# Performance work log

Hardware: AMD Instinct MI355X
Metric: run time of the kernel (lower is better)

The kernel has to match this reference:

```python
import jax, jax.numpy as jnp
import numpy as np

BLOCK = 64       # _aether_cfg['block_size']
JL_DIM = 32      # epsilon_jl_bridge d_out
EPS_GOV = 0.5    # fixed governor eps (governor.target)
ROPE_BASE = 10000.0
RMS_EPS = 1e-6


def _normalize(x, axis=-1):
    n = jnp.sqrt(jnp.sum(x * x, axis=axis, keepdims=True))
    return x / jnp.maximum(n, 1e-12)


def _rms_norm(x):
    return x * jax.lax.rsqrt(jnp.mean(x * x, axis=-1, keepdims=True) + RMS_EPS)


def _rope(x, cos, sin):
    half = x.shape[-1] // 2
    x1, x2 = x[..., :half], x[..., half:]
    return jnp.concatenate([x1 * cos + x2 * sin, -x1 * sin + x2 * cos], axis=-1)


def setup_inputs() -> dict:
    key = jax.random.key(0)
    ks = jax.random.split(key, 6)
    B, S, Dm, H = 2, 2048, 2048, 16
    sc = 1.0 / np.sqrt(Dm)
    x = jax.random.normal(ks[0], (B, S, Dm), jnp.float32)
    Wq = jax.random.normal(ks[1], (Dm, Dm), jnp.float32) * sc
    Wk = jax.random.normal(ks[2], (Dm, Dm), jnp.float32) * sc
    Wv = jax.random.normal(ks[3], (Dm, Dm), jnp.float32) * sc
    Wo = jax.random.normal(ks[4], (Dm, Dm), jnp.float32) * sc
    q_gain = jnp.ones((H,), jnp.float32)
    return {"x": x, "Wq": Wq, "Wk": Wk, "Wv": Wv, "Wo": Wo, "q_gain": q_gain}


def reference(x, Wq, Wk, Wv, Wo, q_gain):
    B, S, Dm = x.shape
    H = q_gain.shape[0]
    Dh = Dm // H

    # QKV projections (bias-free linear, torch weight layout [out,in])
    q = (x @ Wq.T).reshape(B, S, H, Dh).transpose(0, 2, 1, 3)  # (B,H,S,Dh)
    k = (x @ Wk.T).reshape(B, S, H, Dh).transpose(0, 2, 1, 3)
    v = (x @ Wv.T).reshape(B, S, H, Dh).transpose(0, 2, 1, 3)

    # RoPE tables
    inv_freq = 1.0 / (ROPE_BASE ** (jnp.arange(0, Dh, 2, dtype=jnp.float32) / Dh))
    freqs = jnp.outer(jnp.arange(S, dtype=jnp.float32), inv_freq)  # (S,Dh/2)
    cos = jnp.cos(freqs)[None, None]
    sin = jnp.sin(freqs)[None, None]

    q = _rope(_rms_norm(q), cos, sin) * q_gain[None, :, None, None]
    k = _rope(_rms_norm(k), cos, sin)

    # --- aether sparse SDPA: JL block bounds -> top-k blocks -> gather -> SDPA ---
    N = S // BLOCK  # number of KV blocks (static)
    proj = jax.random.normal(jax.random.key(42), (Dh, JL_DIM), jnp.float32) / np.sqrt(JL_DIM)

    q_proj = _normalize(q.mean(axis=2, keepdims=True) @ proj)          # (B,H,1,JL)
    k_blocks = k.reshape(B, H, N, BLOCK, Dh)
    k_proj = _normalize(k_blocks @ proj)                               # (B,H,N,BLOCK,JL)
    centroids = _normalize(k_proj.mean(axis=3))                        # (B,H,N,JL)
    radii = jnp.clip(
        1.0 - jnp.min(jnp.sum(k_proj * centroids[:, :, :, None, :], axis=-1), axis=-1),
        0.0, 1.0)                                                      # (B,H,N)
    ub = jnp.einsum('bhqj,bhnj->bhqn', q_proj, centroids) + radii[:, :, None, :]
    scores = ub[:, :, 0, :]                                            # (B,H,N)
    # force-include the last two blocks (union in the original code)
    scores = scores.at[:, :, N - 2:].set(jnp.inf)

    n_keep = max(2, int(N * min(1.0, EPS_GOV))) + 2                    # static
    _, top_idx = jax.lax.top_k(scores, n_keep)                         # (B,H,n_keep)
    top_idx = jnp.sort(top_idx, axis=-1)
    idx = (top_idx[..., None] * BLOCK + jnp.arange(BLOCK)).reshape(B, H, -1)  # (B,H,K)

    k_s = jnp.take_along_axis(k, idx[..., None], axis=2)               # (B,H,K,Dh)
    v_s = jnp.take_along_axis(v, idx[..., None], axis=2)

    att = jax.nn.softmax(
        jnp.einsum('bhqd,bhkd->bhqk', q, k_s) / np.sqrt(Dh), axis=-1)  # (B,H,S,K)
    y = jnp.einsum('bhqk,bhkd->bhqd', att, v_s)                        # (B,H,S,Dh)

    y = y.transpose(0, 2, 1, 3).reshape(B, S, Dm)
    return y @ Wo.T
```

## Files before the change

kernel.cpp:

```cpp
#include <hip/hip_runtime.h>
#include <hip/hip_bf16.h>

#define B_ 2
#define S_ 2048
#define DM 2048
#define H_ 16
#define DH 128
#define NBLK 32
#define NKEEP 18
#define BH (B_ * H_)

typedef __attribute__((ext_vector_type(8))) short short8;
typedef __attribute__((ext_vector_type(8))) _Float16 f16x8;
typedef __attribute__((ext_vector_type(4))) _Float16 f16x4;
typedef __attribute__((ext_vector_type(4))) float f32x4;

#define GLOAD16(gp, lp)                                                        \
  __builtin_amdgcn_global_load_lds(                                            \
      (const __attribute__((address_space(1))) unsigned int*)(const void*)(gp),\
      (__attribute__((address_space(3))) unsigned int*)(void*)(lp), 16, 0, 0)

__device__ __forceinline__ unsigned short f32_to_bf16(float f) {
  unsigned u = __float_as_uint(f);
  unsigned r = (u + 0x7fffu + ((u >> 16) & 1u)) >> 16;
  return (unsigned short)r;
}
__device__ __forceinline__ float bf16_to_f32(unsigned short h) {
  return __uint_as_float(((unsigned)h) << 16);
}

__device__ __forceinline__ unsigned rotl32(unsigned x, int r) {
  return (x << r) | (x >> (32 - r));
}

__device__ __forceinline__ float erfinv_f32(float x) {
  float w = -log1pf(-x * x);
  float p;
  if (w < 5.0f) {
    w -= 2.5f;
    p = 2.81022636e-08f;
    p = fmaf(p, w, 3.43273939e-07f);
    p = fmaf(p, w, -3.5233877e-06f);
    p = fmaf(p, w, -4.39150654e-06f);
    p = fmaf(p, w, 0.00021858087f);
    p = fmaf(p, w, -0.00125372503f);
    p = fmaf(p, w, -0.00417768164f);
    p = fmaf(p, w, 0.246640727f);
    p = fmaf(p, w, 1.50140941f);
  } else {
    w = sqrtf(w) - 3.0f;
    p = -0.000200214257f;
    p = fmaf(p, w, 0.000100950558f);
    p = fmaf(p, w, 0.00134934322f);
    p = fmaf(p, w, -0.00367342844f);
    p = fmaf(p, w, 0.00573950773f);
    p = fmaf(p, w, -0.0076224613f);
    p = fmaf(p, w, 0.00943887047f);
    p = fmaf(p, w, 1.00167406f);
    p = fmaf(p, w, 2.83297682f);
  }
  return p * x;
}

__device__ __forceinline__ float bits_to_normal(unsigned b) {
  float f = __uint_as_float((b >> 9) | 0x3f800000u) - 1.0f;
  const float lo = -0.9999999403953552f;
  float u = fmaxf(lo, fmaf(f, 2.0f, lo));
  return 1.4142135623730951f * erfinv_f32(u);
}

__global__ void proj_kernel(float* __restrict__ proj) {
  int i = blockIdx.x * blockDim.x + threadIdx.x;
  if (i >= 4096) return;
  unsigned k0 = 0u, k1 = 42u;
  unsigned k2 = 0x1BD11BDAu ^ k0 ^ k1;
  unsigned x0 = 0u, x1 = (unsigned)i;
  x0 += k0; x1 += k1;
#define QR(r) { x0 += x1; x1 = rotl32(x1, r); x1 ^= x0; }
  QR(13) QR(15) QR(26) QR(6)   x0 += k1; x1 += k2 + 1u;
  QR(17) QR(29) QR(16) QR(24)  x0 += k2; x1 += k0 + 2u;
  QR(13) QR(15) QR(26) QR(6)   x0 += k0; x1 += k1 + 3u;
  QR(17) QR(29) QR(16) QR(24)  x0 += k1; x1 += k2 + 4u;
  QR(13) QR(15) QR(26) QR(6)   x0 += k2; x1 += k0 + 5u;
#undef QR
  proj[i] = bits_to_normal(x0 ^ x1) / 5.656854249492381f;
}

__global__ void rope_table_kernel(float* __restrict__ cosb, float* __restrict__ sinb) {
  int s = blockIdx.x;
  int j = threadIdx.x;
  double e = (double)(2 * j) / 128.0;
  double invf = 1.0 / pow(10000.0, e);
  float freq = (float)s * (float)invf;
  cosb[s * 64 + j] = (float)cos((double)freq);
  sinb[s * 64 + j] = (float)sin((double)freq);
}

__global__ __launch_bounds__(256) void split_x3_kernel(const float* __restrict__ in,
                                                       unsigned short* __restrict__ hi,
                                                       unsigned short* __restrict__ lo,
                                                       _Float16* __restrict__ f16,
                                                       int n4) {
  int i = blockIdx.x * blockDim.x + threadIdx.x;
  if (i >= n4) return;
  float4 v = ((const float4*)in)[i];
  ushort4 hv, lv;
  f16x4 fv;
  hv.x = f32_to_bf16(v.x); lv.x = f32_to_bf16(v.x - bf16_to_f32(hv.x)); fv[0] = (_Float16)v.x;
  hv.y = f32_to_bf16(v.y); lv.y = f32_to_bf16(v.y - bf16_to_f32(hv.y)); fv[1] = (_Float16)v.y;
  hv.z = f32_to_bf16(v.z); lv.z = f32_to_bf16(v.z - bf16_to_f32(hv.z)); fv[2] = (_Float16)v.z;
  hv.w = f32_to_bf16(v.w); lv.w = f32_to_bf16(v.w - bf16_to_f32(hv.w)); fv[3] = (_Float16)v.w;
  ((ushort4*)hi)[i] = hv;
  ((ushort4*)lo)[i] = lv;
  ((f16x4*)f16)[i] = fv;
}

__global__ __launch_bounds__(256) void split_kernel(const float* __restrict__ in,
                                                    unsigned short* __restrict__ hi,
                                                    unsigned short* __restrict__ lo,
                                                    int n4) {
  int i = blockIdx.x * blockDim.x + threadIdx.x;
  if (i >= n4) return;
  float4 v = ((const float4*)in)[i];
  ushort4 hv, lv;
  hv.x = f32_to_bf16(v.x); lv.x = f32_to_bf16(v.x - bf16_to_f32(hv.x));
  hv.y = f32_to_bf16(v.y); lv.y = f32_to_bf16(v.y - bf16_to_f32(hv.y));
  hv.z = f32_to_bf16(v.z); lv.z = f32_to_bf16(v.z - bf16_to_f32(hv.z));
  hv.w = f32_to_bf16(v.w); lv.w = f32_to_bf16(v.w - bf16_to_f32(hv.w));
  ((ushort4*)hi)[i] = hv;
  ((ushort4*)lo)[i] = lv;
}

__global__ __launch_bounds__(256) void split_f16_kernel(const float* __restrict__ in,
                                                        _Float16* __restrict__ f16,
                                                        int n4) {
  int i = blockIdx.x * blockDim.x + threadIdx.x;
  if (i >= n4) return;
  float4 v = ((const float4*)in)[i];
  f16x4 fv;
  fv[0] = (_Float16)v.x; fv[1] = (_Float16)v.y;
  fv[2] = (_Float16)v.z; fv[3] = (_Float16)v.w;
  ((f16x4*)f16)[i] = fv;
}

__global__ __launch_bounds__(512, 2) void mfma_gemm_k_sk(const unsigned short* __restrict__ Ahi,
                                                         const unsigned short* __restrict__ Alo,
                                                         const unsigned short* __restrict__ Whi,
                                                         const unsigned short* __restrict__ Wlo,
                                                         float* __restrict__ kp0,
                                                         float* __restrict__ kp1) {
  __shared__ char smem[131072];
  const int t = threadIdx.x, l = t & 63, w = t >> 6;
  const int lin = blockIdx.z * 128 + blockIdx.y * 8 + blockIdx.x;
  const int swz = (lin & 7) * 32 + (lin >> 3);
  const int kz = swz >> 7;
  const int idx = swz & 127;
  const int n0 = (idx & 7) * 256;
  const int m0 = (idx >> 3) * 256;
  const int kbase = kz * 1024;
  float* C = kz ? kp1 : kp0;
  const int wm = w >> 2, wn = w & 3;
  const int lr = l & 15;
  const int lg8 = (l >> 4) * 8;
  const size_t rstep = (size_t)16 * DM;

  const unsigned short* gAh = Ahi + (size_t)(m0 + w * 32 + lr) * DM + lg8;
  const unsigned short* gAl = Alo + (size_t)(m0 + w * 32 + lr) * DM + lg8;
  const unsigned short* gBh = Whi + (size_t)(n0 + w * 32 + lr) * DM + lg8;
  const unsigned short* gBl = Wlo + (size_t)(n0 + w * 32 + lr) * DM + lg8;

  f32x4 acc[8][4];
#pragma unroll
  for (int i = 0; i < 8; ++i)
#pragma unroll
    for (int j = 0; j < 4; ++j) acc[i][j] = (f32x4){0.f, 0.f, 0.f, 0.f};

  {
    char* base = smem + w * 2048;
    GLOAD16(gAh + kbase, base);
    GLOAD16(gAh + rstep + kbase, base + 1024);
    GLOAD16(gAl + kbase, base + 16384);
    GLOAD16(gAl + rstep + kbase, base + 16384 + 1024);
    GLOAD16(gBh + kbase, base + 32768);
    GLOAD16(gBh + rstep + kbase, base + 32768 + 1024);
    GLOAD16(gBl + kbase, base + 49152);
    GLOAD16(gBl + rstep + kbase, base + 49152 + 1024);
  }
  int cur = 0;

#define KQUAD(q)                                                                        \
  {                                                                                     \
    short8 ah0 = *(const short8*)(buf + (wm * 8 + 2 * (q)) * 1024 + l * 16);            \
    short8 ah1 = *(const short8*)(buf + (wm * 8 + 2 * (q) + 1) * 1024 + l * 16);        \
    short8 al0 = *(const short8*)(buf + 16384 + (wm * 8 + 2 * (q)) * 1024 + l * 16);    \
    short8 al1 = *(const short8*)(buf + 16384 + (wm * 8 + 2 * (q) + 1) * 1024 + l * 16);\
    __builtin_amdgcn_s_setprio(1);                                                      \
    _Pragma("unroll")                                                                   \
    for (int n = 0; n < 4; ++n) {                                                       \
      acc[2 * (q)][n] = __builtin_amdgcn_mfma_f32_16x16x32_bf16(ah0, bh[n], acc[2 * (q)][n], 0, 0, 0); \
      acc[2 * (q)][n] = __builtin_amdgcn_mfma_f32_16x16x32_bf16(ah0, bl[n], acc[2 * (q)][n], 0, 0, 0); \
      acc[2 * (q)][n] = __builtin_amdgcn_mfma_f32_16x16x32_bf16(al0, bh[n], acc[2 * (q)][n], 0, 0, 0); \
    }                                                                                   \
    _Pragma("unroll")                                                                   \
    for (int n = 0; n < 4; ++n) {                                                       \
      acc[2 * (q) + 1][n] = __builtin_amdgcn_mfma_f32_16x16x32_bf16(ah1, bh[n], acc[2 * (q) + 1][n], 0, 0, 0); \
      acc[2 * (q) + 1][n] = __builtin_amdgcn_mfma_f32_16x16x32_bf16(ah1, bl[n], acc[2 * (q) + 1][n], 0, 0, 0); \
      acc[2 * (q) + 1][n] = __builtin_amdgcn_mfma_f32_16x16x32_bf16(al1, bh[n], acc[2 * (q) + 1][n], 0, 0, 0); \
    }                                                                                   \
    __builtin_amdgcn_s_setprio(0);                                                      \
  }

  for (int k0 = kbase; k0 < kbase + 1024; k0 += 32) {
    const bool more = (k0 + 32 < kbase + 1024);
    char* buf = smem + cur * 65536;
    char* nb = smem + (cur ^ 1) * 65536 + w * 2048;
    const int kn = k0 + 32;

    if (more) {
      GLOAD16(gBh + kn, nb + 32768);
      GLOAD16(gBh + rstep + kn, nb + 32768 + 1024);
      asm volatile("s_waitcnt vmcnt(2)" ::: "memory");
    } else {
      asm volatile("s_waitcnt vmcnt(0)" ::: "memory");
    }
    __builtin_amdgcn_s_barrier();

    short8 bh[4], bl[4];
#pragma unroll
    for (int f = 0; f < 4; ++f) {
      bh[f] = *(const short8*)(buf + 32768 + (wn * 4 + f) * 1024 + l * 16);
      bl[f] = *(const short8*)(buf + 49152 + (wn * 4 + f) * 1024 + l * 16);
    }
    KQUAD(0);
    __builtin_amdgcn_s_barrier();

    if (more) {
      GLOAD16(gBl + kn, nb + 49152);
      GLOAD16(gBl + rstep + kn, nb + 49152 + 1024);
    }
    KQUAD(1);
    __builtin_amdgcn_s_barrier();

    if (more) {
      GLOAD16(gAh + kn, nb);
      GLOAD16(gAh + rstep + kn, nb + 1024);
    }
    KQUAD(2);
    __builtin_amdgcn_s_barrier();

    if (more) {
      GLOAD16(gAl + kn, nb + 16384);
      GLOAD16(gAl + rstep + kn, nb + 16384 + 1024);
    }
    KQUAD(3);
    __builtin_amdgcn_s_barrier();

    cur ^= 1;
  }
#undef KQUAD

#pragma unroll
  for (int m = 0; m < 8; ++m) {
    int row0 = m0 + wm * 128 + m * 16 + (l >> 4) * 4;
#pragma unroll
    for (int n = 0; n < 4; ++n) {
      int col = n0 + wn * 64 + n * 16 + (l & 15);
      int h = col >> 7, d = col & 127;
#pragma unroll
      for (int r = 0; r < 4; ++r) {
        int mm = row0 + r;
        int b = mm >> 11, s = mm & (S_ - 1);
        C[(((size_t)(b * H_ + h) * S_) + s) * DH + d] = acc[m][n][r];
      }
    }
  }
}

__global__ __launch_bounds__(512, 2) void mfma_gemm_qv(const _Float16* __restrict__ A,
                                                       const _Float16* __restrict__ W,
                                                       float* __restrict__ Cq,
                                                       _Float16* __restrict__ vt) {
  __shared__ char smem[65536];
  const int t = threadIdx.x, l = t & 63, w = t >> 6;
  const int lin = blockIdx.y * gridDim.x + blockIdx.x;
  const int swz = (lin & 7) * 32 + (lin >> 3);
  const int n0 = (swz & 15) * 256;
  const int m0 = (swz >> 4) * 256;
  const int wm = w >> 2, wn = w & 3;
  const int lr = l & 15;
  const int lg8 = (l >> 4) * 8;
  const size_t rstep = (size_t)16 * DM;

  const _Float16* gA = A + (size_t)(m0 + w * 32 + lr) * DM + lg8;
  const _Float16* gB = W + (size_t)(n0 + w * 32 + lr) * DM + lg8;

  f32x4 acc[8][4];
#pragma unroll
  for (int i = 0; i < 8; ++i)
#pragma unroll
    for (int j = 0; j < 4; ++j) acc[i][j] = (f32x4){0.f, 0.f, 0.f, 0.f};

  {
    char* base = smem + w * 2048;
    GLOAD16(gA, base);
    GLOAD16(gA + rstep, base + 1024);
    GLOAD16(gB, base + 16384);
    GLOAD16(gB + rstep, base + 16384 + 1024);
  }
  int cur = 0;

  for (int k0 = 0; k0 < DM; k0 += 32) {
    const bool more = (k0 + 32 < DM);
    char* buf = smem + cur * 32768;
    char* nb = smem + (cur ^ 1) * 32768 + w * 2048;
    const int kn = k0 + 32;

    if (more) {
      GLOAD16(gA + kn, nb);
      GLOAD16(gA + rstep + kn, nb + 1024);
      asm volatile("s_waitcnt vmcnt(2)" ::: "memory");
    } else {
      asm volatile("s_waitcnt vmcnt(0)" ::: "memory");
    }
    __builtin_amdgcn_s_barrier();

    f16x8 b[4];
#pragma unroll
    for (int j = 0; j < 4; ++j)
      b[j] = *(const f16x8*)(buf + 16384 + (wn * 4 + j) * 1024 + l * 16);
    __builtin_amdgcn_s_setprio(1);
#pragma unroll
    for (int i = 0; i < 4; ++i) {
      f16x8 a = *(const f16x8*)(buf + (wm * 8 + i) * 1024 + l * 16);
#pragma unroll
      for (int j = 0; j < 4; ++j)
        acc[i][j] = __builtin_amdgcn_mfma_f32_16x16x32_f16(a, b[j], acc[i][j], 0, 0, 0);
    }
    __builtin_amdgcn_s_setprio(0);
    __builtin_amdgcn_s_barrier();

    if (more) {
      GLOAD16(gB + kn, nb + 16384);
      GLOAD16(gB + rstep + kn, nb + 16384 + 1024);
    }
    __builtin_amdgcn_s_setprio(1);
#pragma unroll
    for (int i = 4; i < 8; ++i) {
      f16x8 a = *(const f16x8*)(buf + (wm * 8 + i) * 1024 + l * 16);
#pragma unroll
      for (int j = 0; j < 4; ++j)
        acc[i][j] = __builtin_amdgcn_mfma_f32_16x16x32_f16(a, b[j], acc[i][j], 0, 0, 0);
    }
    __builtin_amdgcn_s_setprio(0);
    __builtin_amdgcn_s_barrier();

    cur ^= 1;
  }

#pragma unroll
  for (int m = 0; m < 8; ++m) {
    int row0 = m0 + wm * 128 + m * 16 + (l >> 4) * 4;
#pragma unroll
    for (int n = 0; n < 4; ++n) {
      int col = n0 + wn * 64 + n * 16 + (l & 15);
      if (col < DM) {
        int h = col >> 7, d = col & 127;
#pragma unroll
        for (int r = 0; r < 4; ++r) {
          int mm = row0 + r;
          int b2 = mm >> 11, s = mm & (S_ - 1);
          Cq[(((size_t)(b2 * H_ + h) * S_) + s) * DH + d] = acc[m][n][r];
        }
      } else {
        int vcol = col - DM;
        int h = vcol >> 7, d = vcol & 127;
        int b2 = row0 >> 11, s0 = row0 & (S_ - 1);
        f16x4 vv;
        vv[0] = (_Float16)acc[m][n][0];
        vv[1] = (_Float16)acc[m][n][1];
        vv[2] = (_Float16)acc[m][n][2];
        vv[3] = (_Float16)acc[m][n][3];
        *(f16x4*)(vt + (((size_t)(b2 * H_ + h)) * DH + d) * S_ + s0) = vv;
      }
    }
  }
}

template <int MODE>
__global__ __launch_bounds__(256) void mfma_gemm_f16(const _Float16* __restrict__ A,
                                                     const _Float16* __restrict__ W,
                                                     void* __restrict__ Cout) {
  __shared__ char smem[65536];
  const int t = threadIdx.x, l = t & 63, w = t >> 6;
  const int lin = blockIdx.y * gridDim.x + blockIdx.x;
  const int cpx = (gridDim.x * gridDim.y) >> 3;
  const int swz = (lin & 7) * cpx + (lin >> 3);
  const int n0 = (swz % gridDim.x) * 128;
  const int m0 = (swz / gridDim.x) * 128;
  const int wm = w >> 1, wn = w & 1;
  const int lr = l & 15;
  const int lg8 = (l >> 4) * 8;

  auto STAGE = [&](int k0, int c) {
    char* base = smem + c * 32768;
#pragma unroll
    for (int f0 = 0; f0 < 4; ++f0) {
      int f = w * 4 + f0;
      int rb = f >> 1, kh = f & 1;
      GLOAD16(A + (size_t)(m0 + rb * 16 + lr) * DM + k0 + kh * 32 + lg8,
              base + f * 1024);
      GLOAD16(W + (size_t)(n0 + rb * 16 + lr) * DM + k0 + kh * 32 + lg8,
              base + 16384 + f * 1024);
    }
  };

  f32x4 acc[4][4];
#pragma unroll
  for (int i = 0; i < 4; ++i)
#pragma unroll
    for (int j = 0; j < 4; ++j) acc[i][j] = (f32x4){0.f, 0.f, 0.f, 0.f};

  STAGE(0, 0);
  int cur = 0;

  for (int k0 = 0; k0 < DM; k0 += 64) {
    if (k0 + 64 < DM) {
      STAGE(k0 + 64, cur ^ 1);
      asm volatile("s_waitcnt vmcnt(8)" ::: "memory");
    } else {
      asm volatile("s_waitcnt vmcnt(0)" ::: "memory");
    }
    __builtin_amdgcn_s_barrier();

    char* buf = smem + cur * 32768;
    f16x8 a[4][2], b[4][2];
#pragma unroll
    for (int i = 0; i < 4; ++i)
#pragma unroll
      for (int kh = 0; kh < 2; ++kh) {
        a[i][kh] = *(const f16x8*)(buf + ((wm * 4 + i) * 2 + kh) * 1024 + l * 16);
        b[i][kh] = *(const f16x8*)(buf + 16384 + ((wn * 4 + i) * 2 + kh) * 1024 + l * 16);
      }
    __builtin_amdgcn_s_setprio(1);
#pragma unroll
    for (int i = 0; i < 4; ++i)
#pragma unroll
      for (int j = 0; j < 4; ++j) {
        acc[i][j] = __builtin_amdgcn_mfma_f32_16x16x32_f16(a[i][0], b[j][0], acc[i][j], 0, 0, 0);
        acc[i][j] = __builtin_amdgcn_mfma_f32_16x16x32_f16(a[i][1], b[j][1], acc[i][j], 0, 0, 0);
      }
    __builtin_amdgcn_s_setprio(0);
    __builtin_amdgcn_s_barrier();
    cur ^= 1;
  }

#pragma unroll
  for (int i = 0; i < 4; ++i) {
    int row0 = m0 + wm * 64 + i * 16 + (l >> 4) * 4;
#pragma unroll
    for (int j = 0; j < 4; ++j) {
      int col = n0 + wn * 64 + j * 16 + (l & 15);
      if constexpr (MODE == 1) {
        float* C = (float*)Cout;
#pragma unroll
        for (int r = 0; r < 4; ++r)
          C[(size_t)(row0 + r) * DM + col] = acc[i][j][r];
      }
    }
  }
}

__global__ __launch_bounds__(256) void rmsrope_k_kernel(float* __restrict__ k,
                                                        const float* __restrict__ kp1,
                                                        _Float16* __restrict__ kf,
                                                        const float* __restrict__ cosb,
                                                        const float* __restrict__ sinb) {
  int w = threadIdx.x >> 6;
  int lane = threadIdx.x & 63;
  long r = (long)blockIdx.x * 4 + w;
  float* p = k + r * DH;
  const float* p1 = kp1 + r * DH;
  int s = (int)(r & (S_ - 1));
  float x1 = p[lane] + p1[lane];
  float x2 = p[lane + 64] + p1[lane + 64];
  float ss = fmaf(x1, x1, x2 * x2);
#pragma unroll
  for (int off = 32; off; off >>= 1) ss += __shfl_xor(ss, off);
  float rms = rsqrtf(ss * (1.0f / 128.0f) + 1e-6f);
  float n1 = x1 * rms, n2 = x2 * rms;
  float c = cosb[s * 64 + lane], sn = sinb[s * 64 + lane];
  float o1 = fmaf(n1, c, n2 * sn);
  float o2 = fmaf(-n1, sn, n2 * c);
  p[lane] = o1;
  p[lane + 64] = o2;
  kf[r * DH + lane] = (_Float16)o1;
  kf[r * DH + lane + 64] = (_Float16)o2;
}

__global__ __launch_bounds__(256) void rmsrope_q_kernel(float* __restrict__ q,
                                                        const float* __restrict__ cosb,
                                                        const float* __restrict__ sinb,
                                                        const float* __restrict__ qg) {
  int w = threadIdx.x >> 6;
  int lane = threadIdx.x & 63;
  long r = (long)blockIdx.x * 4 + w;
  float* p = q + r * DH;
  int s = (int)(r & (S_ - 1));
  int h = (int)((r >> 11) & (H_ - 1));
  float x1 = p[lane], x2 = p[lane + 64];
  float ss = fmaf(x1, x1, x2 * x2);
#pragma unroll
  for (int off = 32; off; off >>= 1) ss += __shfl_xor(ss, off);
  float rms = rsqrtf(ss * (1.0f / 128.0f) + 1e-6f);
  float n1 = x1 * rms, n2 = x2 * rms;
  float c = cosb[s * 64 + lane], sn = sinb[s * 64 + lane];
  float g = qg[h];
  float o1 = fmaf(n1, c, n2 * sn) * g;
  float o2 = fmaf(-n1, sn, n2 * c) * g;
  p[lane] = o1;
  p[lane + 64] = o2;
}

__global__ __launch_bounds__(256) void qmean_part_kernel(const float* __restrict__ q,
                                                         float* __restrict__ partial) {
  __shared__ float red[256];
  const int bh = blockIdx.x >> 4, chunk = blockIdx.x & 15;
  const int t = threadIdx.x;
  const int d = t & 127, half = t >> 7;
  const float* qb = q + ((size_t)bh * S_ + chunk * 128 + half * 64) * DH;
  float sum = 0.0f;
#pragma unroll 4
  for (int s = 0; s < 64; ++s) sum += qb[(size_t)s * DH + d];
  red[t] = sum;
  __syncthreads();
  if (t < 128) partial[(size_t)blockIdx.x * 128 + t] = red[t] + red[t + 128];
}

__global__ void qproj_kernel(const float* __restrict__ partial,
                             const float* __restrict__ proj,
                             float* __restrict__ qp) {
  __shared__ float meanq[128];
  __shared__ float qps[32];
  __shared__ float nrm;
  const int bh = blockIdx.x, t = threadIdx.x;
  float s = 0.0f;
#pragma unroll
  for (int c = 0; c < 16; ++c) s += partial[((size_t)bh * 16 + c) * 128 + t];
  meanq[t] = s * (1.0f / 2048.0f);
  __syncthreads();
  if (t < 32) {
    float sum = 0.0f;
    for (int d = 0; d < 128; ++d) sum = fmaf(meanq[d], proj[d * 32 + t], sum);
    qps[t] = sum;
  }
  __syncthreads();
  if (t == 0) {
    float sum = 0.0f;
    for (int j = 0; j < 32; ++j) sum += qps[j] * qps[j];
    nrm = 1.0f / fmaxf(sqrtf(sum), 1e-12f);
  }
  __syncthreads();
  if (t < 32) qp[bh * 32 + t] = qps[t] * nrm;
}

__global__ __launch_bounds__(256) void kscore_kernel(const float* __restrict__ k,
                                                     const float* __restrict__ proj,
                                                     const float* __restrict__ qp,
                                                     float* __restrict__ scores) {
  __shared__ float ps[128][32];
  __shared__ float kp[64][33];
  __shared__ float cent[33];
  __shared__ float nrm;
  const int bh = blockIdx.x >> 5, n = blockIdx.x & 31;
  const int t = threadIdx.x;
  for (int i = t; i < 4096; i += 256) ps[i >> 5][i & 31] = proj[i];
  const float* kn = k + ((size_t)bh * S_ + n * 64) * DH;
  __syncthreads();
  {
    int row = t >> 2, j0 = (t & 3) * 8;
    float accv[8];
#pragma unroll
    for (int jj = 0; jj < 8; ++jj) accv[jj] = 0.0f;
#pragma unroll 4
    for (int d = 0; d < 128; ++d) {
      float kv = kn[(size_t)row * DH + d];
#pragma unroll
      for (int jj = 0; jj < 8; ++jj) accv[jj] = fmaf(kv, ps[d][j0 + jj], accv[jj]);
    }
#pragma unroll
    for (int jj = 0; jj < 8; ++jj) kp[row][j0 + jj] = accv[jj];
  }
  __syncthreads();
  if (t < 64) {
    float sum = 0.0f;
    for (int j = 0; j < 32; ++j) sum += kp[t][j] * kp[t][j];
    float scl = 1.0f / fmaxf(sqrtf(sum), 1e-12f);
    for (int j = 0; j < 32; ++j) kp[t][j] *= scl;
  }
  __syncthreads();
  if (t < 32) {
    float sum = 0.0f;
    for (int r2 = 0; r2 < 64; ++r2) sum += kp[r2][t];
    cent[t] = sum * (1.0f / 64.0f);
  }
  __syncthreads();
  if (t == 0) {
    float sum = 0.0f;
    for (int j = 0; j < 32; ++j) sum += cent[j] * cent[j];
    nrm = 1.0f / fmaxf(sqrtf(sum), 1e-12f);
  }
  __syncthreads();
  if (t < 32) cent[t] *= nrm;
  __syncthreads();
  if (t < 64) {
    float dt = 0.0f;
    for (int j = 0; j < 32; ++j) dt = fmaf(kp[t][j], cent[j], dt);
#pragma unroll
    for (int off = 32; off; off >>= 1) dt = fminf(dt, __shfl_xor(dt, off));
    if (t == 0) {
      float radius = fminf(fmaxf(1.0f - dt, 0.0f), 1.0f);
      float dq = 0.0f;
      for (int j = 0; j < 32; ++j) dq = fmaf(qp[bh * 32 + j], cent[j], dq);
      scores[bh * 32 + n] = dq + radius;
    }
  }
}

__global__ void topk_kernel(const float* __restrict__ scores, int* __restrict__ top_idx) {
  if (threadIdx.x != 0) return;
  const int bh = blockIdx.x;
  float sc[NBLK];
  for (int j = 0; j < NBLK; ++j) sc[j] = scores[bh * 32 + j];
  sc[NBLK - 2] = INFINITY;
  sc[NBLK - 1] = INFINITY;
  int chosen[NKEEP];
  bool used[NBLK];
  for (int j = 0; j < NBLK; ++j) used[j] = false;
  for (int kk = 0; kk < NKEEP; ++kk) {
    int best = -1;
    float bv = 0.0f;
    for (int j = 0; j < NBLK; ++j)
      if (!used[j] && (best < 0 || sc[j] > bv)) { bv = sc[j]; best = j; }
    used[best] = true;
    chosen[kk] = best;
  }
  for (int a = 1; a < NKEEP; ++a) {
    int v2 = chosen[a], b2 = a - 1;
    while (b2 >= 0 && chosen[b2] > v2) { chosen[b2 + 1] = chosen[b2]; --b2; }
    chosen[b2 + 1] = v2;
  }
  for (int a = 0; a < NKEEP; ++a) top_idx[bh * NKEEP + a] = chosen[a];
}

__global__ __launch_bounds__(512, 1) void attn_mfma_kernel(const float* __restrict__ q,
                                                           const _Float16* __restrict__ kf,
                                                           const _Float16* __restrict__ vt,
                                                           const int* __restrict__ top_idx,
                                                           _Float16* __restrict__ yf) {
  __shared__ char lds[83968];
  const int bh = blockIdx.x >> 4;
  const int qt = blockIdx.x & 15;
  const int t = threadIdx.x, l = t & 63, w = t >> 6;
  const int lr = l & 15, lg = l >> 4;
  const float scale = 0.08838834764831843f;

  f16x8 qf[4];
  {
    const float* qbase = q + ((size_t)(bh * S_ + qt * 128 + w * 16 + lr)) * DH + lg * 8;
#pragma unroll
    for (int dc = 0; dc < 4; ++dc) {
      float4 v0 = *(const float4*)(qbase + dc * 32);
      float4 v1 = *(const float4*)(qbase + dc * 32 + 4);
      f16x8 h;
      h[0] = (_Float16)v0.x; h[1] = (_Float16)v0.y; h[2] = (_Float16)v0.z; h[3] = (_Float16)v0.w;
      h[4] = (_Float16)v1.x; h[5] = (_Float16)v1.y; h[6] = (_Float16)v1.z; h[7] = (_Float16)v1.w;
      qf[dc] = h;
    }
  }

  float m_[4] = {-INFINITY, -INFINITY, -INFINITY, -INFINITY};
  float ls[4] = {0.f, 0.f, 0.f, 0.f};
  f32x4 yacc[8];
#pragma unroll
  for (int dt = 0; dt < 8; ++dt) yacc[dt] = (f32x4){0.f, 0.f, 0.f, 0.f};

  char* Pw = lds + 65536 + w * 2304;

  const _Float16* kb0 = kf + (size_t)bh * S_ * DH;
  const _Float16* vb0 = vt + (size_t)bh * DH * S_;
  const int* idxp = top_idx + bh * NKEEP;

  auto STAGE = [&](int blk, int c) {
    char* base = lds + c * 32768;
#pragma unroll
    for (int f0 = 0; f0 < 2; ++f0) {
      int f = w * 2 + f0;
      int kt = f >> 2, dc = f & 3;
      GLOAD16(kb0 + (size_t)(blk * 64 + kt * 16 + lr) * DH + dc * 32 + lg * 8,
              base + f * 1024);
      int K0 = f >> 3, dt = f & 7;
      GLOAD16(vb0 + (size_t)(dt * 16 + lr) * S_ + blk * 64 + K0 * 32 + lg * 8,
              base + 16384 + f * 1024);
    }
  };

  int cur = 0;
  STAGE(idxp[0], 0);

  for (int it = 0; it < NKEEP; ++it) {
    if (it + 1 < NKEEP) {
      STAGE(idxp[it + 1], cur ^ 1);
      asm volatile("s_waitcnt vmcnt(4)" ::: "memory");
    } else {
      asm volatile("s_waitcnt vmcnt(0)" ::: "memory");
    }
    __builtin_amdgcn_s_barrier();
    char* buf = lds + cur * 32768;

    f32x4 sacc[4];
#pragma unroll
    for (int kt = 0; kt < 4; ++kt) sacc[kt] = (f32x4){0.f, 0.f, 0.f, 0.f};
    __builtin_amdgcn_s_setprio(1);
#pragma unroll
    for (int kt = 0; kt < 4; ++kt)
#pragma unroll
      for (int dc = 0; dc < 4; ++dc) {
        f16x8 kfr = *(const f16x8*)(buf + (kt * 4 + dc) * 1024 + l * 16);
        sacc[kt] = __builtin_amdgcn_mfma_f32_16x16x32_f16(qf[dc], kfr, sacc[kt], 0, 0, 0);
      }
    __builtin_amdgcn_s_setprio(0);

    float mt[4];
#pragma unroll
    for (int r = 0; r < 4; ++r) {
      float mv = fmaxf(fmaxf(sacc[0][r], sacc[1][r]), fmaxf(sacc[2][r], sacc[3][r])) * scale;
#pragma unroll
      for (int off = 1; off < 16; off <<= 1) mv = fmaxf(mv, __shfl_xor(mv, off));
      mt[r] = mv;
    }
    float p[4][4];
    bool ok = (mt[0] <= m_[0] + 8.0f) && (mt[1] <= m_[1] + 8.0f) &&
              (mt[2] <= m_[2] + 8.0f) && (mt[3] <= m_[3] + 8.0f);
    if (__all(ok)) {
#pragma unroll
      for (int r = 0; r < 4; ++r) {
        float rs = 0.f;
#pragma unroll
        for (int kt = 0; kt < 4; ++kt) {
          p[kt][r] = __expf(fmaf(sacc[kt][r], scale, -m_[r]));
          rs += p[kt][r];
        }
#pragma unroll
        for (int off = 1; off < 16; off <<= 1) rs += __shfl_xor(rs, off);
        ls[r] += rs;
      }
    } else {
#pragma unroll
      for (int r = 0; r < 4; ++r) {
        float mn = fmaxf(m_[r], mt[r]);
        float corr = __expf(m_[r] - mn);
        float rs = 0.f;
#pragma unroll
        for (int kt = 0; kt < 4; ++kt) {
          p[kt][r] = __expf(fmaf(sacc[kt][r], scale, -mn));
          rs += p[kt][r];
        }
#pragma unroll
        for (int off = 1; off < 16; off <<= 1) rs += __shfl_xor(rs, off);
        ls[r] = ls[r] * corr + rs;
        m_[r] = mn;
#pragma unroll
        for (int dt = 0; dt < 8; ++dt) yacc[dt][r] *= corr;
      }
    }

#pragma unroll
    for (int kt = 0; kt < 4; ++kt)
#pragma unroll
      for (int r = 0; r < 4; ++r)
        *(_Float16*)(Pw + (lg * 4 + r) * 144 + (kt * 16 + lr) * 2) = (_Float16)p[kt][r];

    __builtin_amdgcn_s_setprio(1);
#pragma unroll
    for (int K0 = 0; K0 < 2; ++K0) {
      f16x8 pa = *(const f16x8*)(Pw + lr * 144 + K0 * 64 + lg * 16);
#pragma unroll
      for (int dt = 0; dt < 8; ++dt) {
        f16x8 vf = *(const f16x8*)(buf + 16384 + (K0 * 8 + dt) * 1024 + l * 16);
        yacc[dt] = __builtin_amdgcn_mfma_f32_16x16x32_f16(pa, vf, yacc[dt], 0, 0, 0);
      }
    }
    __builtin_amdgcn_s_setprio(0);

    __builtin_amdgcn_s_barrier();
    cur ^= 1;
  }

  const int b = bh >> 4, h = bh & (H_ - 1);
  float inv[4];
#pragma unroll
  for (int r = 0; r < 4; ++r) inv[r] = 1.0f / ls[r];
#pragma unroll
  for (int r = 0; r < 4; ++r) {
    int srow = qt * 128 + w * 16 + lg * 4 + r;
    size_t off0 = ((size_t)b * S_ + srow) * DM + h * DH + lr;
#pragma unroll
    for (int dt = 0; dt < 8; ++dt)
      yf[off0 + dt * 16] = (_Float16)(yacc[dt][r] * inv[r]);
  }
}

extern "C" void kernel_launch(void* const* d_in, const int* in_sizes, int n_in,
                              void* d_out, int out_size, void* d_ws, size_t ws_size,
                              hipStream_t stream) {
  const float* x  = (const float*)d_in[0];
  const float* Wq = (const float*)d_in[1];
  const float* Wk = (const float*)d_in[2];
  const float* Wv = (const float*)d_in[3];
  const float* Wo = (const float*)d_in[4];
  const float* qg = (const float*)d_in[5];
  float* out = (float*)d_out;

  const size_t NE = (size_t)BH * S_ * DH;
  const size_t WE = (size_t)DM * DM;
  char* p = (char*)d_ws;
  float* q_ws = (float*)p; p += NE * 4;
  float* k_ws = (float*)p; p += NE * 4;
  unsigned short* xhi = (unsigned short*)p; p += NE * 2;
  unsigned short* xlo = (unsigned short*)p; p += NE * 2;
  _Float16* xf16 = (_Float16*)p; p += NE * 2;
  unsigned short* wkhi = (unsigned short*)p; p += WE * 2;
  unsigned short* wklo = (unsigned short*)p; p += WE * 2;
  _Float16* wqv = (_Float16*)p; p += 2 * WE * 2;
  float* cosb = (float*)p; p += (size_t)S_ * 64 * 4;
  float* sinb = (float*)p; p += (size_t)S_ * 64 * 4;
  float* projb = (float*)p; p += 4096 * 4;
  int* idxb = (int*)p; p += BH * NKEEP * 4;
  float* scores = (float*)p; p += BH * NBLK * 4;
  float* qpbuf = (float*)p; p += BH * 32 * 4;
  float* qpart = cosb;
  float* kpart1 = q_ws;
  _Float16* kf16 = (_Float16*)wkhi;
  _Float16* vt = (_Float16*)xlo;
  _Float16* yf16 = (_Float16*)xhi;
  _Float16* wo = wqv;

  const int nx4 = (int)(NE / 4);
  const int nw4 = (int)(WE / 4);

  proj_kernel<<<dim3(16), dim3(256), 0, stream>>>(projb);
  rope_table_kernel<<<dim3(S_), dim3(64), 0, stream>>>(cosb, sinb);
  split_x3_kernel<<<dim3(nx4 / 256), dim3(256), 0, stream>>>(x, xhi, xlo, xf16, nx4);
  split_kernel<<<dim3(nw4 / 256), dim3(256), 0, stream>>>(Wk, wkhi, wklo, nw4);
  split_f16_kernel<<<dim3(nw4 / 256), dim3(256), 0, stream>>>(Wq, wqv, nw4);
  split_f16_kernel<<<dim3(nw4 / 256), dim3(256), 0, stream>>>(Wv, wqv + WE, nw4);

  mfma_gemm_k_sk<<<dim3(8, 16, 2), dim3(512), 0, stream>>>(xhi, xlo, wkhi, wklo,
                                                           k_ws, kpart1);

  rmsrope_k_kernel<<<dim3((BH * S_) / 4), dim3(256), 0, stream>>>(k_ws, kpart1, kf16, cosb, sinb);

  mfma_gemm_qv<<<dim3(16, 16), dim3(512), 0, stream>>>(xf16, wqv, q_ws, vt);

  rmsrope_q_kernel<<<dim3((BH * S_) / 4), dim3(256), 0, stream>>>(q_ws, cosb, sinb, qg);

  qmean_part_kernel<<<dim3(BH * 16), dim3(256), 0, stream>>>(q_ws, qpart);
  qproj_kernel<<<dim3(BH), dim3(128), 0, stream>>>(qpart, projb, qpbuf);
  kscore_kernel<<<dim3(BH * NBLK), dim3(256), 0, stream>>>(k_ws, projb, qpbuf, scores);
  topk_kernel<<<dim3(BH), dim3(64), 0, stream>>>(scores, idxb);

  attn_mfma_kernel<<<dim3(BH * 16), dim3(512), 0, stream>>>(q_ws, kf16, vt, idxb, yf16);

  split_f16_kernel<<<dim3(nw4 / 256), dim3(256), 0, stream>>>(Wo, wo, nw4);
  mfma_gemm_f16<1><<<dim3(16, 32), dim3(256), 0, stream>>>(yf16, wo, out);
}
```

Measured before the change: 454.1 us.

## Halve attention query tile to 64 rows and fuse three weight split kernels

The attention kernel now uses 256-thread blocks handling 64 query rows each, so it launches twice as many workgroups, with each wave staging four K/V fragments per block instead of two. LDS per block shrinks, so more workgroups may fit per CU. The aim is better occupancy and load balance across CUs, at the cost of loading each selected K/V block twice as often overall. Separately, the Wk bf16 hi/lo split and the Wq/Wv f16 conversions are merged into one kernel to cut launch overhead.

```diff
diff --git a/kernel.cpp b/kernel.cpp
--- a/kernel.cpp
+++ b/kernel.cpp
@@ -115,20 +115,40 @@
   ((f16x4*)f16)[i] = fv;
 }
 
-__global__ __launch_bounds__(256) void split_kernel(const float* __restrict__ in,
-                                                    unsigned short* __restrict__ hi,
-                                                    unsigned short* __restrict__ lo,
-                                                    int n4) {
+__global__ __launch_bounds__(256) void split_w3_kernel(const float* __restrict__ wk,
+                                                       const float* __restrict__ wq,
+                                                       const float* __restrict__ wv,
+                                                       unsigned short* __restrict__ khi,
+                                                       unsigned short* __restrict__ klo,
+                                                       _Float16* __restrict__ qf,
+                                                       _Float16* __restrict__ vf,
+                                                       int n4) {
   int i = blockIdx.x * blockDim.x + threadIdx.x;
   if (i >= n4) return;
-  float4 v = ((const float4*)in)[i];
-  ushort4 hv, lv;
-  hv.x = f32_to_bf16(v.x); lv.x = f32_to_bf16(v.x - bf16_to_f32(hv.x));
-  hv.y = f32_to_bf16(v.y); lv.y = f32_to_bf16(v.y - bf16_to_f32(hv.y));
-  hv.z = f32_to_bf16(v.z); lv.z = f32_to_bf16(v.z - bf16_to_f32(hv.z));
-  hv.w = f32_to_bf16(v.w); lv.w = f32_to_bf16(v.w - bf16_to_f32(hv.w));
-  ((ushort4*)hi)[i] = hv;
-  ((ushort4*)lo)[i] = lv;
+  {
+    float4 v = ((const float4*)wk)[i];
+    ushort4 hv, lv;
+    hv.x = f32_to_bf16(v.x); lv.x = f32_to_bf16(v.x - bf16_to_f32(hv.x));
+    hv.y = f32_to_bf16(v.y); lv.y = f32_to_bf16(v.y - bf16_to_f32(hv.y));
+    hv.z = f32_to_bf16(v.z); lv.z = f32_to_bf16(v.z - bf16_to_f32(hv.z));
+    hv.w = f32_to_bf16(v.w); lv.w = f32_to_bf16(v.w - bf16_to_f32(hv.w));
+    ((ushort4*)khi)[i] = hv;
+    ((ushort4*)klo)[i] = lv;
+  }
+  {
+    float4 v = ((const float4*)wq)[i];
+    f16x4 fv;
+    fv[0] = (_Float16)v.x; fv[1] = (_Float16)v.y;
+    fv[2] = (_Float16)v.z; fv[3] = (_Float16)v.w;
+    ((f16x4*)qf)[i] = fv;
+  }
+  {
+    float4 v = ((const float4*)wv)[i];
+    f16x4 fv;
+    fv[0] = (_Float16)v.x; fv[1] = (_Float16)v.y;
+    fv[2] = (_Float16)v.z; fv[3] = (_Float16)v.w;
+    ((f16x4*)vf)[i] = fv;
+  }
 }
 
 __global__ __launch_bounds__(256) void split_f16_kernel(const float* __restrict__ in,
@@ -652,21 +672,21 @@
   for (int a = 0; a < NKEEP; ++a) top_idx[bh * NKEEP + a] = chosen[a];
 }
 
-__global__ __launch_bounds__(512, 1) void attn_mfma_kernel(const float* __restrict__ q,
-                                                           const _Float16* __restrict__ kf,
-                                                           const _Float16* __restrict__ vt,
-                                                           const int* __restrict__ top_idx,
-                                                           _Float16* __restrict__ yf) {
-  __shared__ char lds[83968];
-  const int bh = blockIdx.x >> 4;
-  const int qt = blockIdx.x & 15;
+__global__ __launch_bounds__(256) void attn_mfma_kernel(const float* __restrict__ q,
+                                                        const _Float16* __restrict__ kf,
+                                                        const _Float16* __restrict__ vt,
+                                                        const int* __restrict__ top_idx,
+                                                        _Float16* __restrict__ yf) {
+  __shared__ char lds[74752];
+  const int bh = blockIdx.x >> 5;
+  const int qt = blockIdx.x & 31;
   const int t = threadIdx.x, l = t & 63, w = t >> 6;
   const int lr = l & 15, lg = l >> 4;
   const float scale = 0.08838834764831843f;
 
   f16x8 qf[4];
   {
-    const float* qbase = q + ((size_t)(bh * S_ + qt * 128 + w * 16 + lr)) * DH + lg * 8;
+    const float* qbase = q + ((size_t)(bh * S_ + qt * 64 + w * 16 + lr)) * DH + lg * 8;
 #pragma unroll
     for (int dc = 0; dc < 4; ++dc) {
       float4 v0 = *(const float4*)(qbase + dc * 32);
@@ -693,8 +713,8 @@
   auto STAGE = [&](int blk, int c) {
     char* base = lds + c * 32768;
 #pragma unroll
-    for (int f0 = 0; f0 < 2; ++f0) {
-      int f = w * 2 + f0;
+    for (int f0 = 0; f0 < 4; ++f0) {
+      int f = w * 4 + f0;
       int kt = f >> 2, dc = f & 3;
       GLOAD16(kb0 + (size_t)(blk * 64 + kt * 16 + lr) * DH + dc * 32 + lg * 8,
               base + f * 1024);
@@ -710,7 +730,7 @@
   for (int it = 0; it < NKEEP; ++it) {
     if (it + 1 < NKEEP) {
       STAGE(idxp[it + 1], cur ^ 1);
-      asm volatile("s_waitcnt vmcnt(4)" ::: "memory");
+      asm volatile("s_waitcnt vmcnt(8)" ::: "memory");
     } else {
       asm volatile("s_waitcnt vmcnt(0)" ::: "memory");
     }
@@ -802,7 +822,7 @@
   for (int r = 0; r < 4; ++r) inv[r] = 1.0f / ls[r];
 #pragma unroll
   for (int r = 0; r < 4; ++r) {
-    int srow = qt * 128 + w * 16 + lg * 4 + r;
+    int srow = qt * 64 + w * 16 + lg * 4 + r;
     size_t off0 = ((size_t)b * S_ + srow) * DM + h * DH + lr;
 #pragma unroll
     for (int dt = 0; dt < 8; ++dt)
@@ -851,9 +871,8 @@
   proj_kernel<<<dim3(16), dim3(256), 0, stream>>>(projb);
   rope_table_kernel<<<dim3(S_), dim3(64), 0, stream>>>(cosb, sinb);
   split_x3_kernel<<<dim3(nx4 / 256), dim3(256), 0, stream>>>(x, xhi, xlo, xf16, nx4);
-  split_kernel<<<dim3(nw4 / 256), dim3(256), 0, stream>>>(Wk, wkhi, wklo, nw4);
-  split_f16_kernel<<<dim3(nw4 / 256), dim3(256), 0, stream>>>(Wq, wqv, nw4);
-  split_f16_kernel<<<dim3(nw4 / 256), dim3(256), 0, stream>>>(Wv, wqv + WE, nw4);
+  split_w3_kernel<<<dim3(nw4 / 256), dim3(256), 0, stream>>>(Wk, Wq, Wv, wkhi, wklo,
+                                                             wqv, wqv + WE, nw4);
 
   mfma_gemm_k_sk<<<dim3(8, 16, 2), dim3(512), 0, stream>>>(xhi, xlo, wkhi, wklo,
                                                            k_ws, kpart1);
@@ -869,7 +888,7 @@
   kscore_kernel<<<dim3(BH * NBLK), dim3(256), 0, stream>>>(k_ws, projb, qpbuf, scores);
   topk_kernel<<<dim3(BH), dim3(64), 0, stream>>>(scores, idxb);
 
-  attn_mfma_kernel<<<dim3(BH * 16), dim3(512), 0, stream>>>(q_ws, kf16, vt, idxb, yf16);
+  attn_mfma_kernel<<<dim3(BH * 32), dim3(256), 0, stream>>>(q_ws, kf16, vt, idxb, yf16);
 
   split_f16_kernel<<<dim3(nw4 / 256), dim3(256), 0, stream>>>(Wo, wo, nw4);
   mfma_gemm_f16<1><<<dim3(16, 32), dim3(256), 0, stream>>>(yf16, wo, out);
```

Result: no change. 446.6 us (-1.7%).
